# Kernel tuning notes

Hardware: AMD Instinct MI355X
Metric: run time of the kernel (lower is better)

## Reference

```python
import jax, jax.numpy as jnp
import numpy as np

N = 50000      # nodes
E = 800000     # edges (avg degree 16)
RAW = 128      # raw_dim
HID = 256      # hidden_dim
OUT = 64       # out_dim
K = 4          # n_kernels
PHI = 16       # phi_dim
EPS = 1e-8


def setup_inputs() -> dict:
    key = jax.random.key(0)
    ks = jax.random.split(key, 8)
    h_l = jax.random.normal(ks[0], (N, HID), jnp.float32)
    e_l = jax.random.normal(ks[1], (N, RAW), jnp.float32)
    src = jax.random.randint(ks[2], (E,), 0, N, dtype=jnp.int32)
    dst = jax.random.randint(ks[3], (E,), 0, N, dtype=jnp.int32)
    gain = np.sqrt(2.0)
    W_phi = jax.random.normal(ks[4], (RAW, PHI - 1), jnp.float32) * (gain * np.sqrt(2.0 / (RAW + PHI - 1)))
    W1 = jax.random.normal(ks[5], (HID, RAW), jnp.float32) * np.sqrt(2.0 / (RAW + HID))
    b1 = jnp.zeros((HID,), jnp.float32)
    W2 = jax.random.normal(ks[6], (K * PHI, HID), jnp.float32) * np.sqrt(2.0 / (HID + K * PHI))
    b2 = jnp.zeros((K * PHI,), jnp.float32)
    tilde_phi = jnp.eye(PHI, dtype=jnp.float32)[-K:]       # n_kernels <= phi_dim branch
    W = jax.random.normal(ks[7], (HID, OUT * K), jnp.float32) * (gain * np.sqrt(2.0 / (HID + OUT * K)))
    bias = jnp.zeros((OUT,), jnp.float32)
    return {"h_l": h_l, "e_l": e_l, "src": src, "dst": dst,
            "W_phi": W_phi, "W1": W1, "b1": b1, "W2": W2, "b2": b2,
            "tilde_phi": tilde_phi, "W": W, "bias": bias}


def reference(h_l, e_l, src, dst, W_phi, W1, b1, W2, b2, tilde_phi, W, bias):
    # per-node kernelized features: [N, K, OUT]
    h = (h_l @ W).reshape(N, K, OUT)
    # pseudo-coordinates: [N, PHI-1]
    phi_k = e_l @ W_phi
    # normalized kernel anchors: [K, PHI]
    tilde_norm = tilde_phi / jnp.linalg.norm(tilde_phi, axis=1, keepdims=True)
    # deformation offsets: [N, K, PHI]
    hid = jax.nn.relu(e_l @ W1.T + b1)
    delta_k = (hid @ W2.T + b2).reshape(N, K, PHI)
    delta_ik = tilde_norm[None, :, :] + delta_k            # [N, K, PHI]

    # edge relative position (u_sub_v): [E, PHI-1]
    dist = phi_k[src] - phi_k[dst]
    mask = jnp.all(dist == 0.0, axis=1)                    # self/coincident edges
    dist = jnp.concatenate([dist, mask.astype(dist.dtype)[:, None]], axis=1)  # [E, PHI]
    dist = dist / jnp.clip(jnp.linalg.norm(dist, axis=1, keepdims=True), EPS)

    # per-edge per-kernel attention logit: a_ijk = <dist, delta_ik[dst]>  -> [E, K]
    a = jnp.einsum('ep,ekp->ek', dist, delta_ik[dst])

    # edge_softmax: softmax over incoming edges per destination node
    m = jax.ops.segment_max(a, dst, num_segments=N)        # [N, K]
    ex = jnp.exp(a - m[dst])
    s = jax.ops.segment_sum(ex, dst, num_segments=N)       # [N, K]
    att = ex / s[dst]                                      # [E, K]

    # message passing: u_mul_e then sum over incoming edges
    msg = h[src] * att[:, :, None]                         # [E, K, OUT]
    agg = jax.ops.segment_sum(msg, dst, num_segments=N)    # [N, K, OUT]

    out = agg.sum(axis=1) + bias[None, :]                  # [N, OUT]
    out = out / jnp.clip(jnp.linalg.norm(out, axis=1, keepdims=True), EPS)

    # regularizers
    d2 = ((tilde_norm[:, None, :] - tilde_norm[None, :, :]) ** 2).sum(-1)  # [K, K]
    l_sep = d2.sum() / K                                   # sum_k mean_j ||.||^2
    l_focus = (delta_k ** 2).sum(-1).mean()
    return out, l_sep, l_focus
```

## Files before the change

### kernel.cpp

```cpp
#include <hip/hip_runtime.h>
#include <math.h>

#define NN 50000
#define EE 800000

typedef __attribute__((ext_vector_type(8))) short short8;
typedef __attribute__((ext_vector_type(4))) float f32x4;
typedef __attribute__((ext_vector_type(2))) float f32x2;

__device__ inline float b2f(unsigned u16) {
    union { unsigned i; float f; } v; v.i = (u16 & 0xFFFFu) << 16; return v.f;
}
__device__ inline unsigned short f2b(float f) {
    unsigned u = __float_as_uint(f);
    unsigned r = (u + 0x7FFFu + ((u >> 16) & 1u)) >> 16;
    return (unsigned short)r;
}
__device__ inline unsigned cvt_pk_bf16(float lo, float hi) {
    unsigned r;
    asm("v_cvt_pk_bf16_f32 %0, %1, %2" : "=v"(r) : "v"(lo), "v"(hi));
    return r;
}
__device__ inline void gload16(const unsigned short* g, unsigned short* l) {
    __builtin_amdgcn_global_load_lds(
        (const __attribute__((address_space(1))) void*)g,
        (__attribute__((address_space(3))) void*)l, 16, 0, 0);
}

#define PREP_THREADS (800000 + 65536 + 32768 + 16384 + 2048)

__global__ __launch_bounds__(256) void prep_k(const float* __restrict__ W,
                                              const float* __restrict__ W1,
                                              const float* __restrict__ W2,
                                              const float* __restrict__ W_phi,
                                              const float* __restrict__ tilde_phi,
                                              const int* __restrict__ dst,
                                              unsigned short* __restrict__ W_t,
                                              unsigned short* __restrict__ W1_bf,
                                              unsigned short* __restrict__ W2_bf,
                                              unsigned short* __restrict__ Wphi_t,
                                              int* __restrict__ deg,
                                              int* __restrict__ rank,
                                              float* __restrict__ tnorm,
                                              float* __restrict__ lsep_out) {
    if (blockIdx.x == 0) {
        __shared__ float tn[64];
        int t = threadIdx.x;
        if (t < 64) {
            float v = tilde_phi[t];
            float sq = v * v;
            #pragma unroll
            for (int s = 8; s; s >>= 1) sq += __shfl_xor(sq, s, 16);
            float tnv = v / sqrtf(sq);
            tn[t] = tnv;
            tnorm[t] = tnv;
        }
        __syncthreads();
        if (t == 0) {
            float tot = 0.f;
            for (int a = 0; a < 4; ++a)
                for (int b = 0; b < 4; ++b) {
                    float s2 = 0.f;
                    for (int p = 0; p < 16; ++p) {
                        float df = tn[a * 16 + p] - tn[b * 16 + p];
                        s2 += df * df;
                    }
                    tot += s2;
                }
            lsep_out[0] = tot * 0.25f;
        }
    }
    int i = blockIdx.x * 256 + threadIdx.x;
    if (i < 800000) {
        rank[i] = atomicAdd(&deg[dst[i]], 1);
    } else if (i < 865536) {
        int j = i - 800000;
        int cp = j >> 8, r = j & 255;
        int b = (cp & ~63) | ((cp & 15) * 4) | ((cp >> 4) & 3);
        int ch = b >> 2, k = b & 3;
        W_t[j] = f2b(W[(size_t)r * 256 + (k << 6) + ch]);
    } else if (i < 898304) {
        int j = i - 865536;
        W1_bf[j] = f2b(W1[j]);
    } else if (i < 914688) {
        int j = i - 898304;
        W2_bf[j] = f2b(W2[j]);
    } else if (i < 916736) {
        int j = i - 914688;
        int cp = j >> 7, r = j & 127;
        Wphi_t[j] = (cp < 15) ? f2b(W_phi[(size_t)r * 15 + cp]) : (unsigned short)0;
    }
}

__device__ __forceinline__ void hgemm8_body(unsigned short* lds,
                                            const float* __restrict__ A,
                                            const unsigned short* __restrict__ Bt,
                                            unsigned int* __restrict__ h8w,
                                            int bxm, int bxn) {
    unsigned short* As = lds;
    unsigned short* Bs = lds + 8192;
    const int tid = threadIdx.x;
    const int l = tid & 63, l15 = l & 15, l4 = l >> 4;
    const int w = tid >> 6;
    const int wr = w >> 1, wc = w & 1;
    const int row0 = bxm * 128, col0 = bxn * 128;
    const int wrow = wr * 32, wcol = wc * 64;

    const int r_ = tid >> 2, s_ = tid & 3;
    int gr_ = row0 + r_; if (gr_ >= NN) gr_ = NN - 1;

    auto stage = [&](int buf, int k0) {
        const float* Af = A + (size_t)gr_ * 256 + k0 + s_ * 8;
        float4 f0 = *(const float4*)Af, f1 = *(const float4*)(Af + 4);
        *(uint4*)&As[buf * 4096 + tid * 8] =
            make_uint4(cvt_pk_bf16(f0.x, f0.y), cvt_pk_bf16(f0.z, f0.w),
                       cvt_pk_bf16(f1.x, f1.y), cvt_pk_bf16(f1.z, f1.w));
        gload16(&Bt[(size_t)(col0 + r_) * 256 + k0 + s_ * 8],
                &Bs[buf * 4096 + (tid - l) * 8]);
    };

    f32x4 acc[2][4];
    #pragma unroll
    for (int m = 0; m < 2; ++m)
        #pragma unroll
        for (int n = 0; n < 4; ++n) acc[m][n] = (f32x4){0.f, 0.f, 0.f, 0.f};

    stage(0, 0);
    __syncthreads();
    int cur = 0;
    for (int t = 0; t < 8; ++t) {
        if (t + 1 < 8) stage(cur ^ 1, (t + 1) * 32);
        short8 af[2], bfr[4];
        #pragma unroll
        for (int m = 0; m < 2; ++m)
            af[m] = *(const short8*)&As[cur * 4096 + ((wrow + m * 16 + l15) * 4 + l4) * 8];
        #pragma unroll
        for (int n = 0; n < 4; ++n)
            bfr[n] = *(const short8*)&Bs[cur * 4096 + ((wcol + n * 16 + l15) * 4 + l4) * 8];
        #pragma unroll
        for (int m = 0; m < 2; ++m)
            #pragma unroll
            for (int n = 0; n < 4; ++n)
                acc[m][n] = __builtin_amdgcn_mfma_f32_16x16x32_bf16(af[m], bfr[n], acc[m][n], 0, 0, 0);
        if (t + 1 < 8) __syncthreads();
        cur ^= 1;
    }
    #pragma unroll
    for (int m = 0; m < 2; ++m)
        #pragma unroll
        for (int r = 0; r < 4; ++r) {
            int gr = row0 + wrow + m * 16 + l4 * 4 + r;
            if (gr >= NN) continue;
            unsigned pk = __builtin_amdgcn_cvt_pk_fp8_f32(acc[m][0][r], acc[m][1][r], 0, false);
            pk = __builtin_amdgcn_cvt_pk_fp8_f32(acc[m][2][r], acc[m][3][r], pk, true);
            h8w[(size_t)gr * 64 + ((col0 + wcol) >> 2) + l15] = pk;
        }
}

#define LDPAD 264

__device__ __forceinline__ void hiddelta_body(unsigned short* lds,
                                              const float* __restrict__ e_l,
                                              const unsigned short* __restrict__ W1_bf,
                                              const unsigned short* __restrict__ Wphi_t,
                                              const unsigned short* __restrict__ W2_bf,
                                              const float* __restrict__ b1,
                                              const float* __restrict__ b2,
                                              const float* __restrict__ tnorm,
                                              float* __restrict__ phi,
                                              unsigned short* __restrict__ deltap,
                                              float* __restrict__ lf_part, int bxm) {
    unsigned short* As = lds;
    unsigned short* Bs = lds + 2048;
    unsigned short* Wp = lds + 10240;
    unsigned short* hidL = lds;
    const int tid = threadIdx.x;
    const int l = tid & 63, l15 = l & 15, l4 = l >> 4;
    const int w = tid >> 6;
    const int wr = w >> 1, wc = w & 1;
    const int row0 = bxm * 64;

    if (tid < 256) gload16(&Wphi_t[tid * 8], &Wp[(tid - l) * 8]);

    auto stage = [&](int k0) {
        if (tid < 256) {
            int o = tid, r = o >> 2, s = o & 3;
            int gr = row0 + r; if (gr >= NN) gr = NN - 1;
            const float* Af = e_l + (size_t)gr * 128 + k0 + s * 8;
            float4 f0 = *(const float4*)Af, f1 = *(const float4*)(Af + 4);
            *(uint4*)&As[o * 8] = make_uint4(cvt_pk_bf16(f0.x, f0.y), cvt_pk_bf16(f0.z, f0.w),
                                             cvt_pk_bf16(f1.x, f1.y), cvt_pk_bf16(f1.z, f1.w));
        }
        #pragma unroll
        for (int o = tid; o < 1024; o += 512) {
            int r = o >> 2, s = o & 3;
            gload16(&W1_bf[(size_t)r * 128 + k0 + s * 8], &Bs[(o - l) * 8]);
        }
    };

    f32x4 acc[8], pacc;
    #pragma unroll
    for (int n = 0; n < 8; ++n) acc[n] = (f32x4){0.f, 0.f, 0.f, 0.f};
    pacc = (f32x4){0.f, 0.f, 0.f, 0.f};

    stage(0);
    for (int t = 0; t < 4; ++t) {
        int k0 = t * 32;
        __syncthreads();
        short8 af = *(const short8*)&As[((wr * 16 + l15) * 4 + l4) * 8];
        short8 bfr[8];
        #pragma unroll
        for (int n = 0; n < 8; ++n)
            bfr[n] = *(const short8*)&Bs[((wc * 128 + n * 16 + l15) * 4 + l4) * 8];
        #pragma unroll
        for (int n = 0; n < 8; ++n)
            acc[n] = __builtin_amdgcn_mfma_f32_16x16x32_bf16(af, bfr[n], acc[n], 0, 0, 0);
        if (wc == 1) {
            short8 pf = *(const short8*)&Wp[l15 * 128 + k0 + l4 * 8];
            pacc = __builtin_amdgcn_mfma_f32_16x16x32_bf16(af, pf, pacc, 0, 0, 0);
        }
        if (t + 1 < 4) { __syncthreads(); stage((t + 1) * 32); }
    }

    __syncthreads();
    #pragma unroll
    for (int n = 0; n < 8; ++n) {
        int col = wc * 128 + n * 16 + l15;
        float bv = b1[col];
        #pragma unroll
        for (int r = 0; r < 4; ++r) {
            int row = wr * 16 + l4 * 4 + r;
            hidL[row * LDPAD + col] = f2b(fmaxf(acc[n][r] + bv, 0.f));
        }
    }
    if (wc == 1) {
        #pragma unroll
        for (int r = 0; r < 4; ++r) {
            int gr = row0 + wr * 16 + l4 * 4 + r;
            if (gr < NN) phi[(size_t)gr * 16 + l15] = pacc[r];
        }
    }
    __syncthreads();

    f32x4 acc2[2];
    acc2[0] = (f32x4){0.f, 0.f, 0.f, 0.f};
    acc2[1] = (f32x4){0.f, 0.f, 0.f, 0.f};
    for (int kk = 0; kk < 8; ++kk) {
        int k0 = kk * 32;
        short8 a2 = *(const short8*)&hidL[(wr * 16 + l15) * LDPAD + k0 + l4 * 8];
        #pragma unroll
        for (int n = 0; n < 2; ++n) {
            int col = wc * 32 + n * 16 + l15;
            short8 b2f_ = *(const short8*)&W2_bf[(size_t)col * 256 + k0 + l4 * 8];
            acc2[n] = __builtin_amdgcn_mfma_f32_16x16x32_bf16(a2, b2f_, acc2[n], 0, 0, 0);
        }
    }
    float lf = 0.f;
    #pragma unroll
    for (int n = 0; n < 2; ++n) {
        int gc = wc * 32 + n * 16 + l15;
        float bv = b2[gc], tv = tnorm[gc];
        #pragma unroll
        for (int r = 0; r < 4; ++r) {
            int gr = row0 + wr * 16 + l4 * 4 + r;
            if (gr < NN) {
                float v = acc2[n][r] + bv;
                lf += v * v;
                deltap[(size_t)gr * 64 + gc] = f2b(v + tv);
            }
        }
    }
    #pragma unroll
    for (int s = 32; s; s >>= 1) lf += __shfl_xor(lf, s);
    __syncthreads();
    float* red = (float*)&lds[16896];
    if (l == 0) red[w] = lf;
    __syncthreads();
    if (tid == 0) {
        float t_ = 0.f;
        #pragma unroll
        for (int j = 0; j < 8; ++j) t_ += red[j];
        lf_part[bxm] = t_;
    }
}

__global__ __launch_bounds__(512) void fused3_k(const float* __restrict__ e_l,
                                                const float* __restrict__ h_l,
                                                const unsigned short* __restrict__ W1_bf,
                                                const unsigned short* __restrict__ Wphi_t,
                                                const unsigned short* __restrict__ W_t,
                                                const unsigned short* __restrict__ W2_bf,
                                                const float* __restrict__ b1,
                                                const float* __restrict__ b2,
                                                const float* __restrict__ tnorm,
                                                float* __restrict__ phi,
                                                unsigned int* __restrict__ h8w,
                                                unsigned short* __restrict__ deltap,
                                                float* __restrict__ lf_part,
                                                const int* __restrict__ src,
                                                const int* __restrict__ dst,
                                                const int* __restrict__ rank,
                                                const int* __restrict__ offs,
                                                unsigned short* __restrict__ csr_src) {
    __shared__ __align__(16) unsigned short lds[17408];
    int bx = blockIdx.x;
    if (bx < 782) {
        hgemm8_body(lds, h_l, W_t, h8w, bx >> 1, bx & 1);
    } else if (bx < 1564) {
        hiddelta_body(lds, e_l, W1_bf, Wphi_t, W2_bf, b1, b2, tnorm,
                      phi, deltap, lf_part, bx - 782);
    } else {
        int base = (bx - 1564) * 2048 + threadIdx.x;
        int pos[4], sv[4];
        #pragma unroll
        for (int j = 0; j < 4; ++j) {
            int e = base + j * 512;
            if (e < EE) { pos[j] = offs[dst[e]] + rank[e]; sv[j] = src[e]; }
            else pos[j] = -1;
        }
        #pragma unroll
        for (int j = 0; j < 4; ++j)
            if (pos[j] >= 0) csr_src[pos[j]] = (unsigned short)sv[j];
    }
}

#define SCAN_NB ((NN + 255) / 256)
#define LF_NB 782

__global__ __launch_bounds__(256) void scan_partial_k(const int* __restrict__ deg,
                                                      int* __restrict__ bsum) {
    __shared__ int ws_[4];
    int i = blockIdx.x * 256 + threadIdx.x;
    int v = (i < NN) ? deg[i] : 0;
    int x = v;
    #pragma unroll
    for (int s = 32; s; s >>= 1) x += __shfl_xor(x, s);
    if ((threadIdx.x & 63) == 0) ws_[threadIdx.x >> 6] = x;
    __syncthreads();
    if (threadIdx.x == 0) bsum[blockIdx.x] = ws_[0] + ws_[1] + ws_[2] + ws_[3];
}

__global__ __launch_bounds__(256) void scan_bsum_k(int* __restrict__ bsum) {
    __shared__ int sd[256];
    int t = threadIdx.x;
    int v = (t < SCAN_NB) ? bsum[t] : 0;
    sd[t] = v;
    __syncthreads();
    for (int s = 1; s < 256; s <<= 1) {
        int u = (t >= s) ? sd[t - s] : 0;
        __syncthreads();
        sd[t] += u;
        __syncthreads();
    }
    if (t < SCAN_NB) bsum[t] = sd[t] - v;
}

__global__ __launch_bounds__(256) void scan_scatter_k(const int* __restrict__ deg,
                                                      const int* __restrict__ bsum,
                                                      int* __restrict__ offs,
                                                      unsigned short* __restrict__ csr_dst) {
    __shared__ int wexc[4];
    int i = blockIdx.x * 256 + threadIdx.x;
    int lane = threadIdx.x & 63, wid = threadIdx.x >> 6;
    int v = (i < NN) ? deg[i] : 0;
    int x = v;
    #pragma unroll
    for (int d = 1; d < 64; d <<= 1) { int u = __shfl_up(x, d); if (lane >= d) x += u; }
    if (lane == 63) wexc[wid] = x;
    __syncthreads();
    if (threadIdx.x == 0) {
        int a = wexc[0], b = wexc[1], c = wexc[2];
        wexc[0] = 0; wexc[1] = a; wexc[2] = a + b; wexc[3] = a + b + c;
    }
    __syncthreads();
    int excl = (x - v) + wexc[wid] + bsum[blockIdx.x];
    if (i < NN) {
        offs[i + 1] = excl + v;
        if (i == 0) offs[0] = 0;
        for (int q = excl; q < excl + v; ++q) csr_dst[q] = (unsigned short)i;
    }
}

__global__ __launch_bounds__(256) void edge_w_k(const unsigned short* __restrict__ csr_src,
                                                const unsigned short* __restrict__ csr_dst,
                                                const float* __restrict__ phi,
                                                const unsigned short* __restrict__ deltap,
                                                uint2* __restrict__ csr_wb,
                                                const float* __restrict__ lfocus_part,
                                                float* __restrict__ lfocus_out) {
    if (blockIdx.x == 3125) {
        __shared__ float red[4];
        float s = 0.f;
        for (int i = threadIdx.x; i < LF_NB; i += 256) s += lfocus_part[i];
        #pragma unroll
        for (int st = 32; st; st >>= 1) s += __shfl_xor(s, st);
        if ((threadIdx.x & 63) == 0) red[threadIdx.x >> 6] = s;
        __syncthreads();
        if (threadIdx.x == 0)
            lfocus_out[0] = (red[0] + red[1] + red[2] + red[3]) * (1.f / ((float)NN * 4));
        return;
    }
    int e = blockIdx.x * 256 + threadIdx.x;
    if (e >= EE) return;
    int s = csr_src[e], d = csr_dst[e];
    const float4* ps4 = (const float4*)(phi + (size_t)s * 16);
    const float4* pd4 = (const float4*)(phi + (size_t)d * 16);
    float dv[16];
    float nrm2 = 0.f;
    #pragma unroll
    for (int q = 0; q < 4; ++q) {
        float4 a = ps4[q], b = pd4[q];
        dv[q * 4 + 0] = a.x - b.x;
        dv[q * 4 + 1] = a.y - b.y;
        dv[q * 4 + 2] = a.z - b.z;
        dv[q * 4 + 3] = a.w - b.w;
    }
    #pragma unroll
    for (int p = 0; p < 15; ++p) nrm2 += dv[p] * dv[p];
    float z = (nrm2 == 0.f) ? 1.f : 0.f;
    dv[15] = z;
    nrm2 += z;
    float inv = 1.f / fmaxf(sqrtf(nrm2), 1e-8f);
    const uint2* dl2 = (const uint2*)(deltap + (size_t)d * 64);
    float res[4];
    #pragma unroll
    for (int k = 0; k < 4; ++k) {
        float sacc = 0.f;
        #pragma unroll
        for (int q = 0; q < 4; ++q) {
            uint2 u = dl2[k * 4 + q];
            sacc += dv[q * 4 + 0] * b2f(u.x) + dv[q * 4 + 1] * b2f(u.x >> 16)
                  + dv[q * 4 + 2] * b2f(u.y) + dv[q * 4 + 3] * b2f(u.y >> 16);
        }
        res[k] = __expf(sacc * inv);
    }
    csr_wb[e] = make_uint2(cvt_pk_bf16(res[0], res[1]), cvt_pk_bf16(res[2], res[3]));
}

__global__ __launch_bounds__(256) void aggregate_k(const int* __restrict__ offs,
                                                   const unsigned short* __restrict__ csr_src,
                                                   const unsigned int* __restrict__ csr_wu,
                                                   const unsigned int* __restrict__ h8,
                                                   const float* __restrict__ bias,
                                                   float* __restrict__ out) {
    int wave = threadIdx.x >> 6;
    int lane = threadIdx.x & 63;
    int n = blockIdx.x * 4 + wave;
    if (n >= NN) return;
    int beg = offs[n], end = offs[n + 1];

    float pA = 0.f, pB = 0.f;
    for (int q = beg * 2 + lane; q < end * 2; q += 64) {
        unsigned u = csr_wu[q];
        pA += b2f(u);
        pB += b2f(u >> 16);
    }
    #pragma unroll
    for (int s = 2; s < 64; s <<= 1) { pA += __shfl_xor(pA, s); pB += __shfl_xor(pB, s); }
    float iA = (pA > 0.f) ? 1.f / pA : 0.f;
    float iB = (pB > 0.f) ? 1.f / pB : 0.f;
    float i0 = __shfl(iA, 0), i1 = __shfl(iB, 0);
    float i2 = __shfl(iA, 1), i3 = __shfl(iB, 1);

    const uint2* csr_w2 = (const uint2*)csr_wu;
    float a0 = 0.f, a1 = 0.f, a2 = 0.f, a3 = 0.f;
    int p = beg;
    for (; p + 3 < end; p += 4) {
        uint2 u0 = csr_w2[p], u1 = csr_w2[p + 1], u2 = csr_w2[p + 2], u3 = csr_w2[p + 3];
        int s0 = csr_src[p], s1 = csr_src[p + 1], s2 = csr_src[p + 2], s3 = csr_src[p + 3];
        unsigned hv0 = h8[(size_t)s0 * 64 + lane];
        unsigned hv1 = h8[(size_t)s1 * 64 + lane];
        unsigned hv2 = h8[(size_t)s2 * 64 + lane];
        unsigned hv3 = h8[(size_t)s3 * 64 + lane];
        f32x2 lo, hi;
        lo = __builtin_amdgcn_cvt_pk_f32_fp8(hv0, false);
        hi = __builtin_amdgcn_cvt_pk_f32_fp8(hv0, true);
        a0 += b2f(u0.x) * lo.x; a1 += b2f(u0.x >> 16) * lo.y;
        a2 += b2f(u0.y) * hi.x; a3 += b2f(u0.y >> 16) * hi.y;
        lo = __builtin_amdgcn_cvt_pk_f32_fp8(hv1, false);
        hi = __builtin_amdgcn_cvt_pk_f32_fp8(hv1, true);
        a0 += b2f(u1.x) * lo.x; a1 += b2f(u1.x >> 16) * lo.y;
        a2 += b2f(u1.y) * hi.x; a3 += b2f(u1.y >> 16) * hi.y;
        lo = __builtin_amdgcn_cvt_pk_f32_fp8(hv2, false);
        hi = __builtin_amdgcn_cvt_pk_f32_fp8(hv2, true);
        a0 += b2f(u2.x) * lo.x; a1 += b2f(u2.x >> 16) * lo.y;
        a2 += b2f(u2.y) * hi.x; a3 += b2f(u2.y >> 16) * hi.y;
        lo = __builtin_amdgcn_cvt_pk_f32_fp8(hv3, false);
        hi = __builtin_amdgcn_cvt_pk_f32_fp8(hv3, true);
        a0 += b2f(u3.x) * lo.x; a1 += b2f(u3.x >> 16) * lo.y;
        a2 += b2f(u3.y) * hi.x; a3 += b2f(u3.y >> 16) * hi.y;
    }
    for (; p < end; ++p) {
        uint2 uA = csr_w2[p];
        int sA = csr_src[p];
        unsigned hv = h8[(size_t)sA * 64 + lane];
        f32x2 lo = __builtin_amdgcn_cvt_pk_f32_fp8(hv, false);
        f32x2 hi = __builtin_amdgcn_cvt_pk_f32_fp8(hv, true);
        a0 += b2f(uA.x) * lo.x; a1 += b2f(uA.x >> 16) * lo.y;
        a2 += b2f(uA.y) * hi.x; a3 += b2f(uA.y >> 16) * hi.y;
    }
    float v = a0 * i0 + a1 * i1 + a2 * i2 + a3 * i3 + bias[lane];
    float nr = v * v;
    #pragma unroll
    for (int s = 32; s; s >>= 1) nr += __shfl_xor(nr, s);
    float invn = 1.f / fmaxf(sqrtf(nr), 1e-8f);
    out[(size_t)n * 64 + lane] = v * invn;
}

extern "C" void kernel_launch(void* const* d_in, const int* in_sizes, int n_in,
                              void* d_out, int out_size, void* d_ws, size_t ws_size,
                              hipStream_t stream) {
    const float* h_l       = (const float*)d_in[0];
    const float* e_l       = (const float*)d_in[1];
    const int*   src       = (const int*)d_in[2];
    const int*   dst       = (const int*)d_in[3];
    const float* W_phi     = (const float*)d_in[4];
    const float* W1        = (const float*)d_in[5];
    const float* b1        = (const float*)d_in[6];
    const float* W2        = (const float*)d_in[7];
    const float* b2        = (const float*)d_in[8];
    const float* tilde_phi = (const float*)d_in[9];
    const float* W         = (const float*)d_in[10];
    const float* bias      = (const float*)d_in[11];
    float* out = (float*)d_out;
    float* lsep_ptr   = out + (size_t)NN * 64;
    float* lfocus_ptr = out + (size_t)NN * 64 + 1;

    char* ws = (char*)d_ws;
    size_t off = 0;
    auto alloc = [&](size_t bytes) -> char* {
        char* p = ws + off;
        off += (bytes + 255) & ~(size_t)255;
        return p;
    };
    float*          phi     = (float*)alloc((size_t)NN * 16 * 4);
    unsigned short* deltap  = (unsigned short*)alloc((size_t)NN * 64 * 2);
    unsigned int*   h8w     = (unsigned int*)alloc((size_t)NN * 256);
    unsigned short* csr_src = (unsigned short*)alloc((size_t)EE * 2);
    unsigned short* csr_dst = (unsigned short*)alloc((size_t)EE * 2);
    int*            rank    = (int*)alloc((size_t)EE * 4);
    uint2*          csr_wb  = (uint2*)alloc((size_t)EE * 8);
    int*            deg     = (int*)alloc((size_t)NN * 4);
    int*            offs    = (int*)alloc((size_t)(NN + 1) * 4);
    int*            bsum    = (int*)alloc((size_t)SCAN_NB * 4);
    float*          lf_part = (float*)alloc((size_t)LF_NB * 4);
    unsigned short* W_t     = (unsigned short*)alloc(256 * 256 * 2);
    unsigned short* W1_bf   = (unsigned short*)alloc(256 * 128 * 2);
    unsigned short* W2_bf   = (unsigned short*)alloc(64 * 256 * 2);
    unsigned short* Wphi_t  = (unsigned short*)alloc(16 * 128 * 2);
    float*          tnorm   = (float*)alloc(64 * 4);

    hipMemsetAsync(deg, 0, (size_t)NN * 4, stream);

    prep_k<<<(PREP_THREADS + 255) / 256, 256, 0, stream>>>(
        W, W1, W2, W_phi, tilde_phi, dst,
        W_t, W1_bf, W2_bf, Wphi_t, deg, rank, tnorm, lsep_ptr);

    scan_partial_k<<<SCAN_NB, 256, 0, stream>>>(deg, bsum);
    scan_bsum_k<<<1, 256, 0, stream>>>(bsum);
    scan_scatter_k<<<SCAN_NB, 256, 0, stream>>>(deg, bsum, offs, csr_dst);

    fused3_k<<<1955, 512, 0, stream>>>(e_l, h_l, W1_bf, Wphi_t, W_t, W2_bf,
                                       b1, b2, tnorm, phi, h8w, deltap, lf_part,
                                       src, dst, rank, offs, csr_src);

    edge_w_k<<<3126, 256, 0, stream>>>(csr_src, csr_dst, phi, deltap, csr_wb,
                                       lf_part, lfocus_ptr);

    aggregate_k<<<12500, 256, 0, stream>>>(offs, csr_src, (const unsigned int*)csr_wb,
                                           h8w, bias, out);
}
```

Measured before the change: 164.4 us.

## Split fused GEMM kernel, retile h GEMM to 64x256, store phi as bf16

Splits the fused multi-role kernel into a separate h-GEMM kernel, which also does the CSR source scatter, and a separate hidden/delta kernel. The h GEMM is retiled from 128x128 to 64-row by full 256-column blocks with single-buffered LDS and smaller shared memory, so each block reads its A rows once. phi is stored as bf16 instead of fp32 to halve the gather traffic in the edge-weight kernel. In exchange it adds a kernel launch, loses the double-buffered prefetch in the GEMM, and lowers phi precision, which can affect the zero-distance mask test.

```diff
diff --git a/kernel.cpp b/kernel.cpp
--- a/kernel.cpp
+++ b/kernel.cpp
@@ -92,31 +92,53 @@
     }
 }
 
-__device__ __forceinline__ void hgemm8_body(unsigned short* lds,
-                                            const float* __restrict__ A,
-                                            const unsigned short* __restrict__ Bt,
-                                            unsigned int* __restrict__ h8w,
-                                            int bxm, int bxn) {
+__global__ __launch_bounds__(512) void hgemm_k(const float* __restrict__ A,
+                                               const unsigned short* __restrict__ Bt,
+                                               unsigned int* __restrict__ h8w,
+                                               const int* __restrict__ src,
+                                               const int* __restrict__ dst,
+                                               const int* __restrict__ rank,
+                                               const int* __restrict__ offs,
+                                               unsigned short* __restrict__ csr_src) {
+    __shared__ __align__(16) unsigned short lds[10240];
+    int bx = blockIdx.x;
+    if (bx >= 782) {
+        int base = (bx - 782) * 2048 + threadIdx.x;
+        int pos[4], sv[4];
+        #pragma unroll
+        for (int j = 0; j < 4; ++j) {
+            int e = base + j * 512;
+            if (e < EE) { pos[j] = offs[dst[e]] + rank[e]; sv[j] = src[e]; }
+            else pos[j] = -1;
+        }
+        #pragma unroll
+        for (int j = 0; j < 4; ++j)
+            if (pos[j] >= 0) csr_src[pos[j]] = (unsigned short)sv[j];
+        return;
+    }
     unsigned short* As = lds;
-    unsigned short* Bs = lds + 8192;
+    unsigned short* Bs = lds + 2048;
     const int tid = threadIdx.x;
     const int l = tid & 63, l15 = l & 15, l4 = l >> 4;
     const int w = tid >> 6;
-    const int wr = w >> 1, wc = w & 1;
-    const int row0 = bxm * 128, col0 = bxn * 128;
+    const int wr = w >> 2, wc = w & 3;
+    const int row0 = bx * 64;
     const int wrow = wr * 32, wcol = wc * 64;
 
-    const int r_ = tid >> 2, s_ = tid & 3;
-    int gr_ = row0 + r_; if (gr_ >= NN) gr_ = NN - 1;
-
-    auto stage = [&](int buf, int k0) {
-        const float* Af = A + (size_t)gr_ * 256 + k0 + s_ * 8;
-        float4 f0 = *(const float4*)Af, f1 = *(const float4*)(Af + 4);
-        *(uint4*)&As[buf * 4096 + tid * 8] =
-            make_uint4(cvt_pk_bf16(f0.x, f0.y), cvt_pk_bf16(f0.z, f0.w),
-                       cvt_pk_bf16(f1.x, f1.y), cvt_pk_bf16(f1.z, f1.w));
-        gload16(&Bt[(size_t)(col0 + r_) * 256 + k0 + s_ * 8],
-                &Bs[buf * 4096 + (tid - l) * 8]);
+    auto stage = [&](int k0) {
+        if (tid < 256) {
+            int r = tid >> 2, s = tid & 3;
+            int gr = row0 + r; if (gr >= NN) gr = NN - 1;
+            const float* Af = A + (size_t)gr * 256 + k0 + s * 8;
+            float4 f0 = *(const float4*)Af, f1 = *(const float4*)(Af + 4);
+            *(uint4*)&As[tid * 8] = make_uint4(cvt_pk_bf16(f0.x, f0.y), cvt_pk_bf16(f0.z, f0.w),
+                                               cvt_pk_bf16(f1.x, f1.y), cvt_pk_bf16(f1.z, f1.w));
+        }
+        #pragma unroll
+        for (int o = tid; o < 1024; o += 512) {
+            int r = o >> 2, s = o & 3;
+            gload16(&Bt[(size_t)r * 256 + k0 + s * 8], &Bs[(o - l) * 8]);
+        }
     };
 
     f32x4 acc[2][4];
@@ -125,25 +147,22 @@
         #pragma unroll
         for (int n = 0; n < 4; ++n) acc[m][n] = (f32x4){0.f, 0.f, 0.f, 0.f};
 
-    stage(0, 0);
-    __syncthreads();
-    int cur = 0;
+    stage(0);
     for (int t = 0; t < 8; ++t) {
-        if (t + 1 < 8) stage(cur ^ 1, (t + 1) * 32);
+        __syncthreads();
         short8 af[2], bfr[4];
         #pragma unroll
         for (int m = 0; m < 2; ++m)
-            af[m] = *(const short8*)&As[cur * 4096 + ((wrow + m * 16 + l15) * 4 + l4) * 8];
+            af[m] = *(const short8*)&As[((wrow + m * 16 + l15) * 4 + l4) * 8];
         #pragma unroll
         for (int n = 0; n < 4; ++n)
-            bfr[n] = *(const short8*)&Bs[cur * 4096 + ((wcol + n * 16 + l15) * 4 + l4) * 8];
+            bfr[n] = *(const short8*)&Bs[((wcol + n * 16 + l15) * 4 + l4) * 8];
         #pragma unroll
         for (int m = 0; m < 2; ++m)
             #pragma unroll
             for (int n = 0; n < 4; ++n)
                 acc[m][n] = __builtin_amdgcn_mfma_f32_16x16x32_bf16(af[m], bfr[n], acc[m][n], 0, 0, 0);
-        if (t + 1 < 8) __syncthreads();
-        cur ^= 1;
+        if (t + 1 < 8) { __syncthreads(); stage((t + 1) * 32); }
     }
     #pragma unroll
     for (int m = 0; m < 2; ++m)
@@ -153,23 +172,23 @@
             if (gr >= NN) continue;
             unsigned pk = __builtin_amdgcn_cvt_pk_fp8_f32(acc[m][0][r], acc[m][1][r], 0, false);
             pk = __builtin_amdgcn_cvt_pk_fp8_f32(acc[m][2][r], acc[m][3][r], pk, true);
-            h8w[(size_t)gr * 64 + ((col0 + wcol) >> 2) + l15] = pk;
+            h8w[(size_t)gr * 64 + wc * 16 + l15] = pk;
         }
 }
 
 #define LDPAD 264
 
-__device__ __forceinline__ void hiddelta_body(unsigned short* lds,
-                                              const float* __restrict__ e_l,
-                                              const unsigned short* __restrict__ W1_bf,
-                                              const unsigned short* __restrict__ Wphi_t,
-                                              const unsigned short* __restrict__ W2_bf,
-                                              const float* __restrict__ b1,
-                                              const float* __restrict__ b2,
-                                              const float* __restrict__ tnorm,
-                                              float* __restrict__ phi,
-                                              unsigned short* __restrict__ deltap,
-                                              float* __restrict__ lf_part, int bxm) {
+__global__ __launch_bounds__(512) void hiddelta_k(const float* __restrict__ e_l,
+                                                  const unsigned short* __restrict__ W1_bf,
+                                                  const unsigned short* __restrict__ Wphi_t,
+                                                  const unsigned short* __restrict__ W2_bf,
+                                                  const float* __restrict__ b1,
+                                                  const float* __restrict__ b2,
+                                                  const float* __restrict__ tnorm,
+                                                  unsigned short* __restrict__ phi_b,
+                                                  unsigned short* __restrict__ deltap,
+                                                  float* __restrict__ lf_part) {
+    __shared__ __align__(16) unsigned short lds[17408];
     unsigned short* As = lds;
     unsigned short* Bs = lds + 2048;
     unsigned short* Wp = lds + 10240;
@@ -178,6 +197,7 @@
     const int l = tid & 63, l15 = l & 15, l4 = l >> 4;
     const int w = tid >> 6;
     const int wr = w >> 1, wc = w & 1;
+    const int bxm = blockIdx.x;
     const int row0 = bxm * 64;
 
     if (tid < 256) gload16(&Wphi_t[tid * 8], &Wp[(tid - l) * 8]);
@@ -237,7 +257,7 @@
         #pragma unroll
         for (int r = 0; r < 4; ++r) {
             int gr = row0 + wr * 16 + l4 * 4 + r;
-            if (gr < NN) phi[(size_t)gr * 16 + l15] = pacc[r];
+            if (gr < NN) phi_b[(size_t)gr * 16 + l15] = f2b(pacc[r]);
         }
     }
     __syncthreads();
@@ -281,46 +301,6 @@
         #pragma unroll
         for (int j = 0; j < 8; ++j) t_ += red[j];
         lf_part[bxm] = t_;
-    }
-}
-
-__global__ __launch_bounds__(512) void fused3_k(const float* __restrict__ e_l,
-                                                const float* __restrict__ h_l,
-                                                const unsigned short* __restrict__ W1_bf,
-                                                const unsigned short* __restrict__ Wphi_t,
-                                                const unsigned short* __restrict__ W_t,
-                                                const unsigned short* __restrict__ W2_bf,
-                                                const float* __restrict__ b1,
-                                                const float* __restrict__ b2,
-                                                const float* __restrict__ tnorm,
-                                                float* __restrict__ phi,
-                                                unsigned int* __restrict__ h8w,
-                                                unsigned short* __restrict__ deltap,
-                                                float* __restrict__ lf_part,
-                                                const int* __restrict__ src,
-                                                const int* __restrict__ dst,
-                                                const int* __restrict__ rank,
-                                                const int* __restrict__ offs,
-                                                unsigned short* __restrict__ csr_src) {
-    __shared__ __align__(16) unsigned short lds[17408];
-    int bx = blockIdx.x;
-    if (bx < 782) {
-        hgemm8_body(lds, h_l, W_t, h8w, bx >> 1, bx & 1);
-    } else if (bx < 1564) {
-        hiddelta_body(lds, e_l, W1_bf, Wphi_t, W2_bf, b1, b2, tnorm,
-                      phi, deltap, lf_part, bx - 782);
-    } else {
-        int base = (bx - 1564) * 2048 + threadIdx.x;
-        int pos[4], sv[4];
-        #pragma unroll
-        for (int j = 0; j < 4; ++j) {
-            int e = base + j * 512;
-            if (e < EE) { pos[j] = offs[dst[e]] + rank[e]; sv[j] = src[e]; }
-            else pos[j] = -1;
-        }
-        #pragma unroll
-        for (int j = 0; j < 4; ++j)
-            if (pos[j] >= 0) csr_src[pos[j]] = (unsigned short)sv[j];
     }
 }
 
@@ -383,7 +363,7 @@
 
 __global__ __launch_bounds__(256) void edge_w_k(const unsigned short* __restrict__ csr_src,
                                                 const unsigned short* __restrict__ csr_dst,
-                                                const float* __restrict__ phi,
+                                                const unsigned short* __restrict__ phi_b,
                                                 const unsigned short* __restrict__ deltap,
                                                 uint2* __restrict__ csr_wb,
                                                 const float* __restrict__ lfocus_part,
@@ -403,20 +383,26 @@
     int e = blockIdx.x * 256 + threadIdx.x;
     if (e >= EE) return;
     int s = csr_src[e], d = csr_dst[e];
-    const float4* ps4 = (const float4*)(phi + (size_t)s * 16);
-    const float4* pd4 = (const float4*)(phi + (size_t)d * 16);
+    float pv[16], qv[16];
+    {
+        const uint4* P = (const uint4*)(phi_b + (size_t)s * 16);
+        uint4 x0 = P[0], x1 = P[1];
+        unsigned xs[8] = {x0.x, x0.y, x0.z, x0.w, x1.x, x1.y, x1.z, x1.w};
+        #pragma unroll
+        for (int j = 0; j < 8; ++j) { pv[2 * j] = b2f(xs[j]); pv[2 * j + 1] = b2f(xs[j] >> 16); }
+        const uint4* Q = (const uint4*)(phi_b + (size_t)d * 16);
+        uint4 y0 = Q[0], y1 = Q[1];
+        unsigned ys[8] = {y0.x, y0.y, y0.z, y0.w, y1.x, y1.y, y1.z, y1.w};
+        #pragma unroll
+        for (int j = 0; j < 8; ++j) { qv[2 * j] = b2f(ys[j]); qv[2 * j + 1] = b2f(ys[j] >> 16); }
+    }
     float dv[16];
     float nrm2 = 0.f;
     #pragma unroll
-    for (int q = 0; q < 4; ++q) {
-        float4 a = ps4[q], b = pd4[q];
-        dv[q * 4 + 0] = a.x - b.x;
-        dv[q * 4 + 1] = a.y - b.y;
-        dv[q * 4 + 2] = a.z - b.z;
-        dv[q * 4 + 3] = a.w - b.w;
-    }
-    #pragma unroll
-    for (int p = 0; p < 15; ++p) nrm2 += dv[p] * dv[p];
+    for (int p = 0; p < 15; ++p) {
+        dv[p] = pv[p] - qv[p];
+        nrm2 += dv[p] * dv[p];
+    }
     float z = (nrm2 == 0.f) ? 1.f : 0.f;
     dv[15] = z;
     nrm2 += z;
@@ -533,7 +519,7 @@
         off += (bytes + 255) & ~(size_t)255;
         return p;
     };
-    float*          phi     = (float*)alloc((size_t)NN * 16 * 4);
+    unsigned short* phi_b   = (unsigned short*)alloc((size_t)NN * 16 * 2);
     unsigned short* deltap  = (unsigned short*)alloc((size_t)NN * 64 * 2);
     unsigned int*   h8w     = (unsigned int*)alloc((size_t)NN * 256);
     unsigned short* csr_src = (unsigned short*)alloc((size_t)EE * 2);
@@ -560,11 +546,12 @@
     scan_bsum_k<<<1, 256, 0, stream>>>(bsum);
     scan_scatter_k<<<SCAN_NB, 256, 0, stream>>>(deg, bsum, offs, csr_dst);
 
-    fused3_k<<<1955, 512, 0, stream>>>(e_l, h_l, W1_bf, Wphi_t, W_t, W2_bf,
-                                       b1, b2, tnorm, phi, h8w, deltap, lf_part,
-                                       src, dst, rank, offs, csr_src);
-
-    edge_w_k<<<3126, 256, 0, stream>>>(csr_src, csr_dst, phi, deltap, csr_wb,
+    hgemm_k<<<1173, 512, 0, stream>>>(h_l, W_t, h8w, src, dst, rank, offs, csr_src);
+
+    hiddelta_k<<<782, 512, 0, stream>>>(e_l, W1_bf, Wphi_t, W2_bf, b1, b2, tnorm,
+                                        phi_b, deltap, lf_part);
+
+    edge_w_k<<<3126, 256, 0, stream>>>(csr_src, csr_dst, phi_b, deltap, csr_wb,
                                        lf_part, lfocus_ptr);
 
     aggregate_k<<<12500, 256, 0, stream>>>(offs, csr_src, (const unsigned int*)csr_wb,
```

New measurement: 168.5 us. 2.5% more time.
